# Performance work log

Hardware: AMD Instinct MI355X
Metric: run time of the kernel (lower is better)

Reference implementation:

```python
import jax, jax.numpy as jnp
import numpy as np

HARRIS_K = 0.04
SOBEL_SCALE = 1.0 / 12.0  # OpenCV: 1/((1<<(ksize-1))*blockSize) = 1/(4*3) for float input
THRESH_FRAC = 0.7

_DX = jnp.array([[-1., 0., 1.], [-2., 0., 2.], [-1., 0., 1.]], dtype=jnp.float32)
_DY = _DX.T
_BOX = jnp.ones((3, 3), dtype=jnp.float32)  # unnormalized 3x3 box sum (blockSize=3)


def _filt3(img, k):
    # img: (N,1,H,W); reflect-101 pad (OpenCV BORDER_DEFAULT) then valid cross-correlation
    p = jnp.pad(img, ((0, 0), (0, 0), (1, 1), (1, 1)), mode='reflect')
    return jax.lax.conv_general_dilated(
        p, k.reshape(1, 1, 3, 3), (1, 1), 'VALID',
        dimension_numbers=('NCHW', 'OIHW', 'NCHW'))


def harris_mask(x):
    # x: (B,C,H,W) -> binary-ish corner mask, same shape
    B, C, H, W = x.shape
    img = x.reshape(B * C, 1, H, W)
    dx = _filt3(img, _DX) * SOBEL_SCALE
    dy = _filt3(img, _DY) * SOBEL_SCALE
    ixx = _filt3(dx * dx, _BOX)
    ixy = _filt3(dx * dy, _BOX)
    iyy = _filt3(dy * dy, _BOX)
    R = (ixx * iyy - ixy * ixy) - HARRIS_K * (ixx + iyy) ** 2
    # cv2.dilate(dst, None): 3x3 max filter (border does not contribute)
    dst = jax.lax.reduce_window(R, -jnp.inf, jax.lax.max,
                                (1, 1, 3, 3), (1, 1, 1, 1), 'SAME')
    t = THRESH_FRAC * jnp.max(dst, axis=(2, 3), keepdims=True)
    # >t -> 1, <t -> 0, ==t -> keep original pixel (exactly as the torch code does)
    mask = jnp.where(dst > t, 1.0, jnp.where(dst < t, 0.0, img))
    return mask.reshape(B, C, H, W)


def setup_inputs() -> dict:
    key = jax.random.key(0)
    k1, k2, k3 = jax.random.split(key, 3)
    B, C, H, W = 8, 64, 256, 256
    x = jax.random.normal(k1, (B, C, H, W), dtype=jnp.float32)
    weight = jax.random.normal(k2, (C, C, 1, 1), dtype=jnp.float32) * (1.0 / np.sqrt(C))
    bias = jax.random.normal(k3, (C,), dtype=jnp.float32) * 0.01
    return {"x": x, "weight": weight, "bias": bias}


def reference(x, weight, bias):
    # y = ReLU(Conv1x1(x))
    y = jax.lax.conv_general_dilated(
        x, weight, (1, 1), 'VALID',
        dimension_numbers=('NCHW', 'OIHW', 'NCHW')) + bias[None, :, None, None]
    y = jax.nn.relu(y)
    att = harris_mask(x)  # computed via numpy in original -> no grad path
    return att * y + x
```

## Files before the change

### kernel.cpp

```cpp
#include <hip/hip_runtime.h>

#define HH 256
#define WW 256
#define BATCH 8
#define CH 64
#define NIMG (BATCH*CH)
#define HWSZ (HH*WW)
#define SCL (1.0f/12.0f)
#define KH 0.04f
#define TFRAC 0.7f
#define RS 16
#define NEGINF (-__builtin_inff())

__device__ __forceinline__ unsigned encf(float f) {
    unsigned u = __float_as_uint(f);
    return (u & 0x80000000u) ? ~u : (u | 0x80000000u);
}
__device__ __forceinline__ float decf(unsigned u) {
    return __uint_as_float((u & 0x80000000u) ? (u & 0x7fffffffu) : ~u);
}

__global__ __launch_bounds__(256) void k1(const float* __restrict__ x,
                                          float* __restrict__ rv,
                                          unsigned* __restrict__ ms)
{
    const int tid = threadIdx.x;
    const int img = blockIdx.x >> 2;
    const int tx  = tid & 63;
    const int sy  = ((blockIdx.x & 3) << 2) | (tid >> 6);
    const int r0  = sy * RS;
    const int c0  = tx * 4;
    const float* ib = x + (size_t)img * HWSZ;
    float* rb = rv + (size_t)img * HWSZ;

    float im[3][8];
    float px[3][6], pq[3][6], py[3][6];
    float R[3][4];
    float rmax = NEGINF;

    auto loadrow = [&](int gr, float* d) {
        gr = gr < 0 ? -gr : (gr >= HH ? 2*HH - 2 - gr : gr);
        const float* rp = ib + gr * WW;
        float4 own = *(const float4*)(rp + c0);
        float4 lf  = (tx > 0)  ? *(const float4*)(rp + c0 - 4) : own;
        float4 rt  = (tx < 63) ? *(const float4*)(rp + c0 + 4) : own;
        d[0] = (tx > 0)  ? lf.z : own.z;
        d[1] = (tx > 0)  ? lf.w : own.y;
        d[2] = own.x; d[3] = own.y; d[4] = own.z; d[5] = own.w;
        d[6] = (tx < 63) ? rt.x : own.z;
        d[7] = (tx < 63) ? rt.y : own.y;
    };

    loadrow(r0 - 3, im[0]);
    loadrow(r0 - 2, im[1]);

#pragma unroll
    for (int i = 0; i < RS + 4; ++i) {
        const int m = r0 - 2 + i;
        loadrow(m + 1, im[(2 + i) % 3]);

        {
            const int ia = i % 3, ib2 = (i + 1) % 3, ic = (i + 2) % 3;
            float t1[8], t2[8];
#pragma unroll
            for (int q = 0; q < 8; ++q) {
                t1[q] = im[ia][q] + 2.0f * im[ib2][q] + im[ic][q];
                t2[q] = im[ic][q] - im[ia][q];
            }
            const int po = i % 3;
#pragma unroll
            for (int q = 0; q < 6; ++q) {
                float dx = SCL * (t1[q + 2] - t1[q]);
                float dy = SCL * (t2[q] + 2.0f * t2[q + 1] + t2[q + 2]);
                px[po][q] = dx * dx;
                pq[po][q] = dx * dy;
                py[po][q] = dy * dy;
            }
            if (tx == 0)  pq[po][0] = -pq[po][0];
            if (tx == 63) pq[po][5] = -pq[po][5];
        }

        if (i >= 2) {
            const int s = m - 1;
            const int A = (i + 1) % 3, B2 = (i + 2) % 3, C2 = i % 3;
            float Sxx[6], Sxy[6], Syy[6];
            if (s == 0) {
#pragma unroll
                for (int q = 0; q < 6; ++q) {
                    Sxx[q] = px[B2][q] + 2.0f * px[C2][q];
                    Sxy[q] = pq[B2][q] + 2.0f * pq[C2][q];
                    Syy[q] = py[B2][q] + 2.0f * py[C2][q];
                }
            } else if (s == HH - 1) {
#pragma unroll
                for (int q = 0; q < 6; ++q) {
                    Sxx[q] = 2.0f * px[A][q] + px[B2][q];
                    Sxy[q] = 2.0f * pq[A][q] + pq[B2][q];
                    Syy[q] = 2.0f * py[A][q] + py[B2][q];
                }
            } else {
#pragma unroll
                for (int q = 0; q < 6; ++q) {
                    Sxx[q] = px[A][q] + px[B2][q] + px[C2][q];
                    Sxy[q] = pq[A][q] + pq[B2][q] + pq[C2][q];
                    Syy[q] = py[A][q] + py[B2][q] + py[C2][q];
                }
            }
            const bool vs = (s >= 0) && (s < HH);
#pragma unroll
            for (int j = 0; j < 4; ++j) {
                float ixx = Sxx[j] + Sxx[j + 1] + Sxx[j + 2];
                float ixy = Sxy[j] + Sxy[j + 1] + Sxy[j + 2];
                float iyy = Syy[j] + Syy[j + 1] + Syy[j + 2];
                float tr = ixx + iyy;
                float Rj = (ixx * iyy - ixy * ixy) - KH * tr * tr;
                Rj = vs ? Rj : NEGINF;
                R[i % 3][j] = Rj;
                rmax = fmaxf(rmax, Rj);
            }
        }

        if (i >= 4) {
            const int r = r0 - 4 + i;
            const int A = (i + 1) % 3, B2 = (i + 2) % 3, C2 = i % 3;
            float4 o;
            o.x = fmaxf(fmaxf(R[A][0], R[B2][0]), R[C2][0]);
            o.y = fmaxf(fmaxf(R[A][1], R[B2][1]), R[C2][1]);
            o.z = fmaxf(fmaxf(R[A][2], R[B2][2]), R[C2][2]);
            o.w = fmaxf(fmaxf(R[A][3], R[B2][3]), R[C2][3]);
            *(float4*)(rb + r * WW + c0) = o;
        }
    }

#pragma unroll
    for (int off = 32; off; off >>= 1) rmax = fmaxf(rmax, __shfl_xor(rmax, off));
    __shared__ float sm[4];
    if ((tid & 63) == 0) sm[tid >> 6] = rmax;
    __syncthreads();
    if (tid == 0) {
        float mm = fmaxf(fmaxf(sm[0], sm[1]), fmaxf(sm[2], sm[3]));
        atomicMax(ms + img, encf(mm));
    }
}

__global__ __launch_bounds__(512, 4) void k2(const float* __restrict__ x,
                                             const float* __restrict__ wgt,
                                             const float* __restrict__ bias,
                                             const unsigned* __restrict__ ms,
                                             float* __restrict__ io)
{
    __shared__ __align__(16) float Xl[CH][WW];
    __shared__ __align__(16) float Wl[CH][CH];
    const int tid = threadIdx.x;
    const int wv  = tid >> 6;
    const int l   = tid & 63;
    const int b   = blockIdx.x >> 8;
    const int h   = blockIdx.x & 255;
    const int oc0 = wv << 3;

    {
        const float* xrow = x + (size_t)b * CH * HWSZ + (size_t)h * WW + (l << 2);
        float4 tmp[8];
#pragma unroll
        for (int k = 0; k < 8; ++k)
            tmp[k] = *(const float4*)(xrow + (size_t)(oc0 + k) * HWSZ);
#pragma unroll
        for (int k = 0; k < 8; ++k)
            *(float4*)&Xl[oc0 + k][l << 2] = tmp[k];

        const float4* wg4 = (const float4*)wgt;
        float4* wl4 = (float4*)&Wl[0][0];
        float4 w0 = wg4[tid], w1 = wg4[tid + 512];
        wl4[tid] = w0; wl4[tid + 512] = w1;
    }
    __syncthreads();

    float acc[8][4];
#pragma unroll
    for (int j = 0; j < 8; ++j) {
        const float bj = bias[oc0 + j];
        acc[j][0] = bj; acc[j][1] = bj; acc[j][2] = bj; acc[j][3] = bj;
    }
#pragma unroll 4
    for (int c2 = 0; c2 < CH; c2 += 2) {
        const float4 xa = *(const float4*)&Xl[c2][l << 2];
        const float4 xb = *(const float4*)&Xl[c2 + 1][l << 2];
#pragma unroll
        for (int j = 0; j < 8; ++j) {
            const float2 wj = *(const float2*)&Wl[oc0 + j][c2];
            acc[j][0] = fmaf(wj.x, xa.x, acc[j][0]);
            acc[j][1] = fmaf(wj.x, xa.y, acc[j][1]);
            acc[j][2] = fmaf(wj.x, xa.z, acc[j][2]);
            acc[j][3] = fmaf(wj.x, xa.w, acc[j][3]);
            acc[j][0] = fmaf(wj.y, xb.x, acc[j][0]);
            acc[j][1] = fmaf(wj.y, xb.y, acc[j][1]);
            acc[j][2] = fmaf(wj.y, xb.z, acc[j][2]);
            acc[j][3] = fmaf(wj.y, xb.w, acc[j][3]);
        }
    }

    const size_t pb = (size_t)b * CH * HWSZ + (size_t)h * WW + (size_t)(l << 2);
    float4 rvv[8];
#pragma unroll
    for (int j = 0; j < 8; ++j)
        rvv[j] = *(const float4*)(io + pb + (size_t)(oc0 + j) * HWSZ);

#pragma unroll
    for (int j = 0; j < 8; ++j) {
        const int c = oc0 + j;
        float lf = __shfl_up(rvv[j].w, 1);
        float rt = __shfl_down(rvv[j].x, 1);
        if (l == 0)  lf = NEGINF;
        if (l == 63) rt = NEGINF;
        const float d0 = fmaxf(fmaxf(lf,       rvv[j].x), rvv[j].y);
        const float d1 = fmaxf(fmaxf(rvv[j].x, rvv[j].y), rvv[j].z);
        const float d2 = fmaxf(fmaxf(rvv[j].y, rvv[j].z), rvv[j].w);
        const float d3 = fmaxf(fmaxf(rvv[j].z, rvv[j].w), rt);
        const float t = TFRAC * decf(ms[b * CH + c]);
        const float4 xi = *(const float4*)&Xl[c][l << 2];
        const float y0 = fmaxf(acc[j][0], 0.0f);
        const float y1 = fmaxf(acc[j][1], 0.0f);
        const float y2 = fmaxf(acc[j][2], 0.0f);
        const float y3 = fmaxf(acc[j][3], 0.0f);
        float4 o;
        o.x = fmaf(d0 > t ? 1.0f : (d0 < t ? 0.0f : xi.x), y0, xi.x);
        o.y = fmaf(d1 > t ? 1.0f : (d1 < t ? 0.0f : xi.y), y1, xi.y);
        o.z = fmaf(d2 > t ? 1.0f : (d2 < t ? 0.0f : xi.z), y2, xi.z);
        o.w = fmaf(d3 > t ? 1.0f : (d3 < t ? 0.0f : xi.w), y3, xi.w);
        *(float4*)(io + pb + (size_t)c * HWSZ) = o;
    }
}

extern "C" void kernel_launch(void* const* d_in, const int* in_sizes, int n_in,
                              void* d_out, int out_size, void* d_ws, size_t ws_size,
                              hipStream_t stream)
{
    const float* x    = (const float*)d_in[0];
    const float* wgt  = (const float*)d_in[1];
    const float* bias = (const float*)d_in[2];
    float* out = (float*)d_out;
    unsigned* ms = (unsigned*)d_ws;

    hipMemsetAsync(ms, 0, NIMG * sizeof(unsigned), stream);
    hipLaunchKernelGGL(k1, dim3(NIMG * 4), dim3(256), 0, stream, x, out, ms);
    hipLaunchKernelGGL(k2, dim3(BATCH * HH), dim3(512), 0, stream,
                       x, wgt, bias, ms, out);
}
```

Before: 362.3 us.

## Separate box filter horizontally, shuffle halos, and drop atomic max plus memset

The horizontal 3-tap box sum of the structure-tensor products is now done once per row as each row is produced, which cuts the per-output adds and the number of live registers. Neighbour halo columns come from wavefront shuffles instead of two extra float4 global loads per row. The per-image atomicMax on encoded floats becomes a plain store of four partial maxima per image, which k2 reduces into shared memory. This removes the memset launch and the per-element threshold decode. The risk is extra shuffle latency in the row loader and a slightly different floating-point summation order.

```diff
diff --git a/kernel.cpp b/kernel.cpp
--- a/kernel.cpp
+++ b/kernel.cpp
@@ -12,17 +12,9 @@
 #define RS 16
 #define NEGINF (-__builtin_inff())
 
-__device__ __forceinline__ unsigned encf(float f) {
-    unsigned u = __float_as_uint(f);
-    return (u & 0x80000000u) ? ~u : (u | 0x80000000u);
-}
-__device__ __forceinline__ float decf(unsigned u) {
-    return __uint_as_float((u & 0x80000000u) ? (u & 0x7fffffffu) : ~u);
-}
-
 __global__ __launch_bounds__(256) void k1(const float* __restrict__ x,
                                           float* __restrict__ rv,
-                                          unsigned* __restrict__ ms)
+                                          float* __restrict__ ms)
 {
     const int tid = threadIdx.x;
     const int img = blockIdx.x >> 2;
@@ -34,21 +26,22 @@
     float* rb = rv + (size_t)img * HWSZ;
 
     float im[3][8];
-    float px[3][6], pq[3][6], py[3][6];
+    float hx[3][4], hq[3][4], hy[3][4];
     float R[3][4];
     float rmax = NEGINF;
 
     auto loadrow = [&](int gr, float* d) {
         gr = gr < 0 ? -gr : (gr >= HH ? 2*HH - 2 - gr : gr);
-        const float* rp = ib + gr * WW;
-        float4 own = *(const float4*)(rp + c0);
-        float4 lf  = (tx > 0)  ? *(const float4*)(rp + c0 - 4) : own;
-        float4 rt  = (tx < 63) ? *(const float4*)(rp + c0 + 4) : own;
-        d[0] = (tx > 0)  ? lf.z : own.z;
-        d[1] = (tx > 0)  ? lf.w : own.y;
+        float4 own = *(const float4*)(ib + gr * WW + c0);
+        float upz = __shfl_up(own.z, 1);
+        float upw = __shfl_up(own.w, 1);
+        float dnx = __shfl_down(own.x, 1);
+        float dny = __shfl_down(own.y, 1);
+        d[0] = (tx > 0)  ? upz : own.z;
+        d[1] = (tx > 0)  ? upw : own.y;
         d[2] = own.x; d[3] = own.y; d[4] = own.z; d[5] = own.w;
-        d[6] = (tx < 63) ? rt.x : own.z;
-        d[7] = (tx < 63) ? rt.y : own.y;
+        d[6] = (tx < 63) ? dnx : own.z;
+        d[7] = (tx < 63) ? dny : own.y;
     };
 
     loadrow(r0 - 3, im[0]);
@@ -67,51 +60,46 @@
                 t1[q] = im[ia][q] + 2.0f * im[ib2][q] + im[ic][q];
                 t2[q] = im[ic][q] - im[ia][q];
             }
-            const int po = i % 3;
+            float pxv[6], pqv[6], pyv[6];
 #pragma unroll
             for (int q = 0; q < 6; ++q) {
                 float dx = SCL * (t1[q + 2] - t1[q]);
                 float dy = SCL * (t2[q] + 2.0f * t2[q + 1] + t2[q + 2]);
-                px[po][q] = dx * dx;
-                pq[po][q] = dx * dy;
-                py[po][q] = dy * dy;
-            }
-            if (tx == 0)  pq[po][0] = -pq[po][0];
-            if (tx == 63) pq[po][5] = -pq[po][5];
+                pxv[q] = dx * dx;
+                pqv[q] = dx * dy;
+                pyv[q] = dy * dy;
+            }
+            if (tx == 0)  pqv[0] = -pqv[0];
+            if (tx == 63) pqv[5] = -pqv[5];
+            const int po = i % 3;
+#pragma unroll
+            for (int j = 0; j < 4; ++j) {
+                hx[po][j] = pxv[j] + pxv[j + 1] + pxv[j + 2];
+                hq[po][j] = pqv[j] + pqv[j + 1] + pqv[j + 2];
+                hy[po][j] = pyv[j] + pyv[j + 1] + pyv[j + 2];
+            }
         }
 
         if (i >= 2) {
             const int s = m - 1;
             const int A = (i + 1) % 3, B2 = (i + 2) % 3, C2 = i % 3;
-            float Sxx[6], Sxy[6], Syy[6];
-            if (s == 0) {
-#pragma unroll
-                for (int q = 0; q < 6; ++q) {
-                    Sxx[q] = px[B2][q] + 2.0f * px[C2][q];
-                    Sxy[q] = pq[B2][q] + 2.0f * pq[C2][q];
-                    Syy[q] = py[B2][q] + 2.0f * py[C2][q];
+            const bool vs = (s >= 0) && (s < HH);
+#pragma unroll
+            for (int j = 0; j < 4; ++j) {
+                float ixx, ixy, iyy;
+                if (s == 0) {
+                    ixx = hx[B2][j] + 2.0f * hx[C2][j];
+                    ixy = hq[B2][j] + 2.0f * hq[C2][j];
+                    iyy = hy[B2][j] + 2.0f * hy[C2][j];
+                } else if (s == HH - 1) {
+                    ixx = 2.0f * hx[A][j] + hx[B2][j];
+                    ixy = 2.0f * hq[A][j] + hq[B2][j];
+                    iyy = 2.0f * hy[A][j] + hy[B2][j];
+                } else {
+                    ixx = hx[A][j] + hx[B2][j] + hx[C2][j];
+                    ixy = hq[A][j] + hq[B2][j] + hq[C2][j];
+                    iyy = hy[A][j] + hy[B2][j] + hy[C2][j];
                 }
-            } else if (s == HH - 1) {
-#pragma unroll
-                for (int q = 0; q < 6; ++q) {
-                    Sxx[q] = 2.0f * px[A][q] + px[B2][q];
-                    Sxy[q] = 2.0f * pq[A][q] + pq[B2][q];
-                    Syy[q] = 2.0f * py[A][q] + py[B2][q];
-                }
-            } else {
-#pragma unroll
-                for (int q = 0; q < 6; ++q) {
-                    Sxx[q] = px[A][q] + px[B2][q] + px[C2][q];
-                    Sxy[q] = pq[A][q] + pq[B2][q] + pq[C2][q];
-                    Syy[q] = py[A][q] + py[B2][q] + py[C2][q];
-                }
-            }
-            const bool vs = (s >= 0) && (s < HH);
-#pragma unroll
-            for (int j = 0; j < 4; ++j) {
-                float ixx = Sxx[j] + Sxx[j + 1] + Sxx[j + 2];
-                float ixy = Sxy[j] + Sxy[j + 1] + Sxy[j + 2];
-                float iyy = Syy[j] + Syy[j + 1] + Syy[j + 2];
                 float tr = ixx + iyy;
                 float Rj = (ixx * iyy - ixy * ixy) - KH * tr * tr;
                 Rj = vs ? Rj : NEGINF;
@@ -139,18 +127,19 @@
     __syncthreads();
     if (tid == 0) {
         float mm = fmaxf(fmaxf(sm[0], sm[1]), fmaxf(sm[2], sm[3]));
-        atomicMax(ms + img, encf(mm));
+        ms[(img << 2) | (blockIdx.x & 3)] = mm;
     }
 }
 
 __global__ __launch_bounds__(512, 4) void k2(const float* __restrict__ x,
                                              const float* __restrict__ wgt,
                                              const float* __restrict__ bias,
-                                             const unsigned* __restrict__ ms,
+                                             const float* __restrict__ ms,
                                              float* __restrict__ io)
 {
     __shared__ __align__(16) float Xl[CH][WW];
     __shared__ __align__(16) float Wl[CH][CH];
+    __shared__ float tmax[CH];
     const int tid = threadIdx.x;
     const int wv  = tid >> 6;
     const int l   = tid & 63;
@@ -172,6 +161,11 @@
         float4* wl4 = (float4*)&Wl[0][0];
         float4 w0 = wg4[tid], w1 = wg4[tid + 512];
         wl4[tid] = w0; wl4[tid + 512] = w1;
+
+        if (tid < CH) {
+            float4 m4 = *(const float4*)(ms + ((b * CH + tid) << 2));
+            tmax[tid] = TFRAC * fmaxf(fmaxf(m4.x, m4.y), fmaxf(m4.z, m4.w));
+        }
     }
     __syncthreads();
 
@@ -216,7 +210,7 @@
         const float d1 = fmaxf(fmaxf(rvv[j].x, rvv[j].y), rvv[j].z);
         const float d2 = fmaxf(fmaxf(rvv[j].y, rvv[j].z), rvv[j].w);
         const float d3 = fmaxf(fmaxf(rvv[j].z, rvv[j].w), rt);
-        const float t = TFRAC * decf(ms[b * CH + c]);
+        const float t = tmax[c];
         const float4 xi = *(const float4*)&Xl[c][l << 2];
         const float y0 = fmaxf(acc[j][0], 0.0f);
         const float y1 = fmaxf(acc[j][1], 0.0f);
@@ -239,9 +233,8 @@
     const float* wgt  = (const float*)d_in[1];
     const float* bias = (const float*)d_in[2];
     float* out = (float*)d_out;
-    unsigned* ms = (unsigned*)d_ws;
-
-    hipMemsetAsync(ms, 0, NIMG * sizeof(unsigned), stream);
+    float* ms = (float*)d_ws;
+
     hipLaunchKernelGGL(k1, dim3(NIMG * 4), dim3(256), 0, stream, x, out, ms);
     hipLaunchKernelGGL(k2, dim3(BATCH * HH), dim3(512), 0, stream,
                        x, wgt, bias, ms, out);
```

After: 329.0 us. 1.1x faster.
